# Performance work log

Hardware: AMD Instinct MI355X
Metric: run time of the kernel (lower is better)

Reference implementation:

```python
import jax, jax.numpy as jnp
import numpy as np

D_MODEL = 1024
NUM_HEADS = 16
DEPTH = D_MODEL // NUM_HEADS  # 64
BATCH = 4
SEQ = 2048


def _split_heads(x, batch):
    # [B, S, d_model] -> [B, H, S, depth]
    x = x.reshape(batch, -1, NUM_HEADS, DEPTH)
    return jnp.transpose(x, (0, 2, 1, 3))


def setup_inputs() -> dict:
    key = jax.random.key(0)
    ks = jax.random.split(key, 8)
    q = jax.random.normal(ks[0], (BATCH, SEQ, D_MODEL), jnp.float32)
    k = jax.random.normal(ks[1], (BATCH, SEQ, D_MODEL), jnp.float32)
    v = jax.random.normal(ks[2], (BATCH, SEQ, D_MODEL), jnp.float32)
    scale = 0.02
    wq = jax.random.normal(ks[3], (D_MODEL, D_MODEL), jnp.float32) * scale
    wk = jax.random.normal(ks[4], (D_MODEL, D_MODEL), jnp.float32) * scale
    wv = jax.random.normal(ks[5], (D_MODEL, D_MODEL), jnp.float32) * scale
    wo = jax.random.normal(ks[6], (D_MODEL, D_MODEL), jnp.float32) * scale
    zeros_b = jnp.zeros((D_MODEL,), jnp.float32)
    ones_mask = jnp.ones((BATCH, SEQ, 1), jnp.float32)
    return {
        "q": q, "k": k, "v": v,
        "query_mask": ones_mask, "key_mask": ones_mask, "value_mask": ones_mask,
        "wq": wq, "bq": zeros_b, "wk": wk, "bk": zeros_b,
        "wv": wv, "bv": zeros_b, "wo": wo, "bo": zeros_b,
    }


def reference(q, k, v, query_mask, key_mask, value_mask,
              wq, bq, wk, bk, wv, bv, wo, bo):
    batch, q_len, _ = q.shape
    # elementwise input masks (multiplicative, as in the original call())
    q = q * query_mask
    k = k * key_mask
    v = v * value_mask
    # linear projections + head split
    qh = _split_heads(q @ wq + bq, batch)  # [B, H, Q, depth]
    kh = _split_heads(k @ wk + bk, batch)  # [B, H, S, depth]
    vh = _split_heads(v @ wv + bv, batch)  # [B, H, S, depth]
    key_len = kh.shape[2]
    layout_length = key_len // NUM_HEADS  # L
    # The TF slice_assign loop uses full slices on every axis, so each
    # iteration overwrites the whole buffer; after the loop only the LAST
    # head-block slice survives. Faithful math:
    start = (NUM_HEADS - 1) * layout_length
    fk = kh[:, :, start:start + layout_length, :]  # [B, H, L, depth]
    fv = vh[:, :, start:start + layout_length, :]  # [B, H, L, depth]
    dk = jnp.asarray(DEPTH, jnp.float32)
    logits = jnp.einsum("bhqd,bhld->bhql", qh, fk) / jnp.sqrt(dk)
    # autoreg mask: 1 - lower_triangular(ones(Q, L)) -> strictly upper masked
    tri = jnp.tril(jnp.ones((q_len, layout_length), jnp.float32))
    mask = (1.0 - tri)[None, None, :, :]
    logits = logits + mask * (-1e9)
    attn = jax.nn.softmax(logits, axis=-1)  # [B, H, Q, L]
    out = jnp.einsum("bhql,bhld->bhqd", attn, fv)  # [B, H, Q, depth]
    out = jnp.transpose(out, (0, 2, 1, 3)).reshape(batch, -1, D_MODEL)
    output = out @ wo + bo
    return (output, attn)
```

## Files before the change

kernel.cpp:

```cpp
#include <hip/hip_runtime.h>

typedef unsigned short u16;
typedef unsigned int u32;
typedef __attribute__((ext_vector_type(8))) short short8;
typedef __attribute__((ext_vector_type(4))) short short4v;
typedef __attribute__((ext_vector_type(4))) float f32x4;

__device__ __forceinline__ u16 f2bf(float f) {
  union { float f; u32 u; } v; v.f = f;
  u32 u = v.u;
  u32 r = (u + 0x7fffu + ((u >> 16) & 1u)) >> 16;
  return (u16)r;
}

__device__ __forceinline__ void async_ld16(const u16* g, u16* l) {
  __builtin_amdgcn_global_load_lds(
      (const __attribute__((address_space(1))) void*)g,
      (__attribute__((address_space(3))) void*)l, 16, 0, 0);
}

__global__ __launch_bounds__(256) void prep(
    const float* __restrict__ q, const float* __restrict__ qm,
    const float* __restrict__ k, const float* __restrict__ km,
    const float* __restrict__ v, const float* __restrict__ vm,
    const float* __restrict__ wq, const float* __restrict__ wk,
    const float* __restrict__ wv, const float* __restrict__ wo,
    u16* __restrict__ Qc, u16* __restrict__ Kc, u16* __restrict__ Vc,
    u16* __restrict__ WqT, u16* __restrict__ WkT, u16* __restrict__ WvT,
    u16* __restrict__ WoT) {
  __shared__ u16 tile[32][33];
  const int bid = blockIdx.x;
  const int tid = threadIdx.x;
  if (bid < 8192) {
    int i = (bid * 256 + tid) * 4;
    float m = qm[i >> 10];
    float4 vv = *(const float4*)(q + i);
    short4v o;
    o.x = (short)f2bf(vv.x * m);
    o.y = (short)f2bf(vv.y * m);
    o.z = (short)f2bf(vv.z * m);
    o.w = (short)f2bf(vv.w * m);
    *(short4v*)(Qc + i) = o;
  } else if (bid < 9216) {
    int zb = bid - 8192;
    int z = zb >> 9;
    int bx = zb & 511;
    const float* src = z ? v : k;
    const float* mask = z ? vm : km;
    u16* dst = z ? Vc : Kc;
    int i = (bx * 256 + tid) * 4;
    int r = i >> 10, c = i & 1023;
    size_t sr = (size_t)(r >> 7) * 2048 + 1920 + (r & 127);
    float m = mask[sr];
    float4 vv = *(const float4*)(src + sr * 1024 + c);
    short4v o;
    o.x = (short)f2bf(vv.x * m);
    o.y = (short)f2bf(vv.y * m);
    o.z = (short)f2bf(vv.z * m);
    o.w = (short)f2bf(vv.w * m);
    *(short4v*)(dst + i) = o;
  } else {
    int idx = bid - 9216;
    int z = idx >> 10;
    int rem = idx & 1023;
    const float* W = (z == 0) ? wq : (z == 1) ? wk : (z == 2) ? wv : wo;
    u16* WT = (z == 0) ? WqT : (z == 1) ? WkT : (z == 2) ? WvT : WoT;
    int tx = tid & 31, ty = tid >> 5;
    int x = (rem & 31) * 32 + tx;
    int y0 = (rem >> 5) * 32;
    for (int i = ty; i < 32; i += 8)
      tile[i][tx] = f2bf(W[(size_t)(y0 + i) * 1024 + x]);
    __syncthreads();
    int x2 = y0 + tx;
    int r0 = (rem & 31) * 32;
    for (int i = ty; i < 32; i += 8)
      WT[(size_t)(r0 + i) * 1024 + x2] = tile[tx][i];
  }
}

template <int OUTMODE>
__device__ __forceinline__ void gemm_body(
    const u16* __restrict__ A, const u16* __restrict__ BT,
    const float* __restrict__ bias, void* __restrict__ Cv, int N, int K,
    int bx, int by) {
  __shared__ u16 As[128 * 32];
  __shared__ u16 Bs[128 * 32];
  const int wave = threadIdx.x >> 6, lane = threadIdx.x & 63;
  const int ln = lane & 15, quad = lane >> 4;
  const int w0 = wave & 1, w1 = wave >> 1;
  const int row0 = bx * 128;
  const int col0 = by * 128;
  const int srow = lane >> 2, scol = (lane & 3) * 8;
  const u16* gA = A + (size_t)(row0 + wave * 32 + srow) * K + scol;
  const u16* gB = BT + (size_t)(col0 + wave * 32 + srow) * K + scol;
  u16* lA = &As[(wave * 32) * 32];
  u16* lB = &Bs[(wave * 32) * 32];

  f32x4 acc[4][4];
  for (int i = 0; i < 4; ++i)
    for (int j = 0; j < 4; ++j) acc[i][j] = f32x4{0.f, 0.f, 0.f, 0.f};

  for (int k0 = 0; k0 < K; k0 += 32) {
    async_ld16(gA + k0, lA);
    async_ld16(gA + (size_t)16 * K + k0, lA + 16 * 32);
    async_ld16(gB + k0, lB);
    async_ld16(gB + (size_t)16 * K + k0, lB + 16 * 32);
    __syncthreads();
    short8 af[4], bf[4];
    for (int mt = 0; mt < 4; ++mt)
      af[mt] = *(const short8*)&As[(w1 * 64 + mt * 16 + ln) * 32 + quad * 8];
    for (int nt = 0; nt < 4; ++nt)
      bf[nt] = *(const short8*)&Bs[(w0 * 64 + nt * 16 + ln) * 32 + quad * 8];
    for (int mt = 0; mt < 4; ++mt)
      for (int nt = 0; nt < 4; ++nt)
        acc[mt][nt] = __builtin_amdgcn_mfma_f32_16x16x32_bf16(af[mt], bf[nt],
                                                              acc[mt][nt], 0, 0, 0);
    __syncthreads();
  }

  for (int nt = 0; nt < 4; ++nt) {
    int c = col0 + w0 * 64 + nt * 16 + ln;
    float bval = bias ? bias[c] : 0.f;
    for (int mt = 0; mt < 4; ++mt)
      for (int reg = 0; reg < 4; ++reg) {
        int r = row0 + w1 * 64 + mt * 16 + quad * 4 + reg;
        float val = acc[mt][nt][reg] + bval;
        if (OUTMODE == 3) {
          ((float*)Cv)[(size_t)r * N + c] = val;
        } else if (OUTMODE == 0) {
          ((u16*)Cv)[(size_t)r * N + c] = f2bf(val);
        } else if (OUTMODE == 1) {
          size_t idx = ((size_t)(r >> 7) << 17) + ((size_t)(c >> 6) << 13) +
                       ((size_t)(r & 127) << 6) + (c & 63);
          ((u16*)Cv)[idx] = f2bf(val);
        } else {
          size_t idx = ((size_t)(r >> 7) << 17) + ((size_t)(c >> 6) << 13) +
                       ((size_t)(c & 63) << 7) + (r & 127);
          ((u16*)Cv)[idx] = f2bf(val);
        }
      }
  }
}

__global__ __launch_bounds__(256) void proj(
    const u16* __restrict__ Qc, const u16* __restrict__ Kc,
    const u16* __restrict__ Vc, const u16* __restrict__ WqT,
    const u16* __restrict__ WkT, const u16* __restrict__ WvT,
    const float* __restrict__ bq, const float* __restrict__ bk,
    const float* __restrict__ bv, u16* __restrict__ Qws, u16* __restrict__ FK,
    u16* __restrict__ FVT) {
  int orig = blockIdx.x;
  int id = (orig & 7) * 72 + (orig >> 3);
  if (id < 512) {
    gemm_body<0>(Qc, WqT, bq, Qws, 1024, 1024, id >> 3, id & 7);
  } else if (id < 544) {
    int t = id - 512;
    gemm_body<1>(Kc, WkT, bk, FK, 1024, 1024, t >> 3, t & 7);
  } else {
    int t = id - 544;
    gemm_body<2>(Vc, WvT, bv, FVT, 1024, 1024, t >> 3, t & 7);
  }
}

__global__ __launch_bounds__(256) void gemm_o(const u16* __restrict__ A,
                                              const u16* __restrict__ BT,
                                              const float* __restrict__ bias,
                                              float* __restrict__ C) {
  int orig = blockIdx.x;
  int id = (orig & 7) * 64 + (orig >> 3);
  gemm_body<3>(A, BT, bias, C, 1024, 1024, id >> 3, id & 7);
}

__global__ __launch_bounds__(256) void attn_kernel(
    const u16* __restrict__ Q, const u16* __restrict__ FK,
    const u16* __restrict__ FVT, float* __restrict__ attn_out,
    u16* __restrict__ OUTP) {
  __shared__ u16 pbuf[4][16 * 136];
  const int wave = threadIdx.x >> 6, lane = threadIdx.x & 63;
  const int ln = lane & 15, quad = lane >> 4;
  const int bh = blockIdx.x, b = bh >> 4, h = bh & 15;
  const int q0 = blockIdx.y * 64 + wave * 16;

  const u16* qp = Q + (size_t)(b * 2048 + q0 + ln) * 1024 + h * 64 + quad * 8;
  const u16* fk = FK + ((size_t)bh << 13);
  const u16* fvt = FVT + ((size_t)bh << 13);

  f32x4 acc[8];
  for (int i = 0; i < 8; ++i) acc[i] = f32x4{0.f, 0.f, 0.f, 0.f};
  for (int ks = 0; ks < 2; ++ks) {
    short8 a = *(const short8*)(qp + ks * 32);
    __builtin_amdgcn_s_setprio(1);
    for (int nt = 0; nt < 8; ++nt) {
      short8 bfrag = *(const short8*)(fk + (size_t)(nt * 16 + ln) * 64 +
                                      ks * 32 + quad * 8);
      acc[nt] = __builtin_amdgcn_mfma_f32_16x16x32_bf16(a, bfrag, acc[nt], 0, 0, 0);
    }
    __builtin_amdgcn_s_setprio(0);
  }
  float mx[4] = {-3e38f, -3e38f, -3e38f, -3e38f};
  for (int nt = 0; nt < 8; ++nt) {
    int l = nt * 16 + ln;
    for (int reg = 0; reg < 4; ++reg) {
      int qg = q0 + quad * 4 + reg;
      float vv = acc[nt][reg] * 0.125f;
      if (l > qg) vv = -1e9f;
      acc[nt][reg] = vv;
      mx[reg] = fmaxf(mx[reg], vv);
    }
  }
  for (int off = 1; off < 16; off <<= 1)
    for (int reg = 0; reg < 4; ++reg)
      mx[reg] = fmaxf(mx[reg], __shfl_xor(mx[reg], off, 64));
  float sm[4] = {0.f, 0.f, 0.f, 0.f};
  for (int nt = 0; nt < 8; ++nt)
    for (int reg = 0; reg < 4; ++reg) {
      float p = __expf(acc[nt][reg] - mx[reg]);
      acc[nt][reg] = p;
      sm[reg] += p;
    }
  for (int off = 1; off < 16; off <<= 1)
    for (int reg = 0; reg < 4; ++reg) sm[reg] += __shfl_xor(sm[reg], off, 64);
  float inv[4];
  for (int reg = 0; reg < 4; ++reg) inv[reg] = 1.f / sm[reg];
  {
    float* ao = attn_out + ((size_t)bh * 2048 + q0 + quad * 4) * 128 + ln;
    u16* pw = &pbuf[wave][(quad * 4) * 136 + ln];
    for (int nt = 0; nt < 8; ++nt)
      for (int reg = 0; reg < 4; ++reg) {
        float pv = acc[nt][reg] * inv[reg];
        ao[(size_t)reg * 128 + nt * 16] = pv;
        pw[reg * 136 + nt * 16] = f2bf(pv);
      }
  }
  f32x4 o[4];
  for (int i = 0; i < 4; ++i) o[i] = f32x4{0.f, 0.f, 0.f, 0.f};
  for (int kk = 0; kk < 4; ++kk) {
    short8 a = *(const short8*)&pbuf[wave][ln * 136 + kk * 32 + quad * 8];
    __builtin_amdgcn_s_setprio(1);
    for (int nt = 0; nt < 4; ++nt) {
      short8 bfrag = *(const short8*)(fvt + (size_t)(nt * 16 + ln) * 128 +
                                      kk * 32 + quad * 8);
      o[nt] = __builtin_amdgcn_mfma_f32_16x16x32_bf16(a, bfrag, o[nt], 0, 0, 0);
    }
    __builtin_amdgcn_s_setprio(0);
  }
  {
    u16* ot = &pbuf[wave][0];
    for (int nt = 0; nt < 4; ++nt)
      for (int reg = 0; reg < 4; ++reg)
        ot[(quad * 4 + reg) * 72 + nt * 16 + ln] = f2bf(o[nt][reg]);
    int row = lane >> 2;
    u16* dst = OUTP + (size_t)(b * 2048 + q0 + row) * 1024 + h * 64;
    for (int p = 0; p < 2; ++p) {
      int col = p * 32 + (lane & 3) * 8;
      *(short8*)(dst + col) = *(const short8*)&ot[row * 72 + col];
    }
  }
}

extern "C" void kernel_launch(void* const* d_in, const int* in_sizes, int n_in,
                              void* d_out, int out_size, void* d_ws,
                              size_t ws_size, hipStream_t stream) {
  const float* q = (const float*)d_in[0];
  const float* k = (const float*)d_in[1];
  const float* v = (const float*)d_in[2];
  const float* qm = (const float*)d_in[3];
  const float* km = (const float*)d_in[4];
  const float* vm = (const float*)d_in[5];
  const float* wq = (const float*)d_in[6];
  const float* bq = (const float*)d_in[7];
  const float* wk = (const float*)d_in[8];
  const float* bk = (const float*)d_in[9];
  const float* wv = (const float*)d_in[10];
  const float* bv = (const float*)d_in[11];
  const float* wo = (const float*)d_in[12];
  const float* bo = (const float*)d_in[13];
  float* out = (float*)d_out;
  float* attn_out = out + (size_t)4 * 2048 * 1024;

  char* ws = (char*)d_ws;
  const size_t MB = 1ull << 20;
  u16* WqT = (u16*)(ws + 0 * MB);
  u16* WkT = (u16*)(ws + 2 * MB);
  u16* WvT = (u16*)(ws + 4 * MB);
  u16* WoT = (u16*)(ws + 6 * MB);
  u16* Qws = (u16*)(ws + 8 * MB);
  u16* FKw = (u16*)(ws + 24 * MB);
  u16* FVTw = (u16*)(ws + 25 * MB);
  u16* OUTP = (u16*)(ws + 26 * MB);
  u16* Qc = OUTP;
  u16* Kc = (u16*)(ws + 42 * MB);
  u16* Vc = (u16*)(ws + 43 * MB);

  prep<<<13312, 256, 0, stream>>>(q, qm, k, km, v, vm, wq, wk, wv, wo, Qc, Kc,
                                  Vc, WqT, WkT, WvT, WoT);
  proj<<<576, 256, 0, stream>>>(Qc, Kc, Vc, WqT, WkT, WvT, bq, bk, bv, Qws,
                                FKw, FVTw);
  attn_kernel<<<dim3(64, 32), 256, 0, stream>>>(Qws, FKw, FVTw, attn_out, OUTP);
  gemm_o<<<512, 256, 0, stream>>>(OUTP, WoT, bo, out);
}
```

Before: 284.6 us.

## Fuse Q projection with attention via LDS tile and atomic flag for K/V readiness

Merges the projection and attention kernels into one launch: each block computes a 128x128 Q-projection tile into shared memory and immediately runs attention for the two heads and 64-row groups it covers, so the Q intermediate never goes through global memory. The first 64 blocks additionally compute the K/V last-slice projections and signal completion through an atomic counter that all blocks spin on. This removes a kernel launch and the Q write/readback, but puts extra serial work on the first 64 blocks. It also relies on all 512 blocks being co-resident or the K/V producers being scheduled first; otherwise the spin-wait can deadlock.

```diff
diff --git a/kernel.cpp b/kernel.cpp
--- a/kernel.cpp
+++ b/kernel.cpp
@@ -82,9 +82,7 @@
 __device__ __forceinline__ void gemm_body(
     const u16* __restrict__ A, const u16* __restrict__ BT,
     const float* __restrict__ bias, void* __restrict__ Cv, int N, int K,
-    int bx, int by) {
-  __shared__ u16 As[128 * 32];
-  __shared__ u16 Bs[128 * 32];
+    int bx, int by, u16* __restrict__ As, u16* __restrict__ Bs) {
   const int wave = threadIdx.x >> 6, lane = threadIdx.x & 63;
   const int ln = lane & 15, quad = lane >> 4;
   const int w0 = wave & 1, w1 = wave >> 1;
@@ -127,38 +125,151 @@
         float val = acc[mt][nt][reg] + bval;
         if (OUTMODE == 3) {
           ((float*)Cv)[(size_t)r * N + c] = val;
-        } else if (OUTMODE == 0) {
-          ((u16*)Cv)[(size_t)r * N + c] = f2bf(val);
         } else if (OUTMODE == 1) {
           size_t idx = ((size_t)(r >> 7) << 17) + ((size_t)(c >> 6) << 13) +
                        ((size_t)(r & 127) << 6) + (c & 63);
           ((u16*)Cv)[idx] = f2bf(val);
-        } else {
+        } else if (OUTMODE == 2) {
           size_t idx = ((size_t)(r >> 7) << 17) + ((size_t)(c >> 6) << 13) +
                        ((size_t)(c & 63) << 7) + (r & 127);
           ((u16*)Cv)[idx] = f2bf(val);
+        } else {
+          ((u16*)Cv)[wave * 4608 + (mt * 16 + quad * 4 + reg) * 72 +
+                     nt * 16 + ln] = f2bf(val);
         }
       }
   }
 }
 
-__global__ __launch_bounds__(256) void proj(
+__global__ __launch_bounds__(256, 2) void proj_attn(
     const u16* __restrict__ Qc, const u16* __restrict__ Kc,
     const u16* __restrict__ Vc, const u16* __restrict__ WqT,
     const u16* __restrict__ WkT, const u16* __restrict__ WvT,
     const float* __restrict__ bq, const float* __restrict__ bk,
-    const float* __restrict__ bv, u16* __restrict__ Qws, u16* __restrict__ FK,
-    u16* __restrict__ FVT) {
-  int orig = blockIdx.x;
-  int id = (orig & 7) * 72 + (orig >> 3);
-  if (id < 512) {
-    gemm_body<0>(Qc, WqT, bq, Qws, 1024, 1024, id >> 3, id & 7);
-  } else if (id < 544) {
-    int t = id - 512;
-    gemm_body<1>(Kc, WkT, bk, FK, 1024, 1024, t >> 3, t & 7);
-  } else {
-    int t = id - 544;
-    gemm_body<2>(Vc, WvT, bv, FVT, 1024, 1024, t >> 3, t & 7);
+    const float* __restrict__ bv, u16* __restrict__ FK, u16* __restrict__ FVT,
+    float* __restrict__ attn_out, u16* __restrict__ OUTP,
+    u32* __restrict__ flags) {
+  __shared__ u16 As[128 * 32];
+  __shared__ u16 Bs[128 * 32];
+  __shared__ u16 qt_s[4 * 4608];
+  __shared__ u16 p_s[4 * 2176];
+  const int bid = blockIdx.x;
+  const int wave = threadIdx.x >> 6, lane = threadIdx.x & 63;
+  const int ln = lane & 15, quad = lane >> 4;
+
+  if (bid < 64) {
+    int z = bid >> 5, t = bid & 31;
+    if (z == 0)
+      gemm_body<1>(Kc, WkT, bk, FK, 1024, 1024, t >> 3, t & 7, As, Bs);
+    else
+      gemm_body<2>(Vc, WvT, bv, FVT, 1024, 1024, t >> 3, t & 7, As, Bs);
+    __syncthreads();
+    __threadfence();
+    if (threadIdx.x == 0)
+      __hip_atomic_fetch_add(flags, 1u, __ATOMIC_RELEASE,
+                             __HIP_MEMORY_SCOPE_AGENT);
+    __syncthreads();
+  }
+
+  int id = (bid & 7) * 64 + (bid >> 3);
+  const int bx = id >> 3, by = id & 7;
+  gemm_body<4>(Qc, WqT, bq, (void*)qt_s, 1024, 1024, bx, by, As, Bs);
+
+  if (threadIdx.x == 0) {
+    while (__hip_atomic_load(flags, __ATOMIC_ACQUIRE,
+                             __HIP_MEMORY_SCOPE_AGENT) < 64u)
+      __builtin_amdgcn_s_sleep(8);
+  }
+  __syncthreads();
+  __threadfence();
+
+  const int w0 = wave & 1, w1 = wave >> 1;
+  const int h = 2 * by + w0;
+  const int rowbase = bx * 128 + w1 * 64;
+  const int b = rowbase >> 11, q0 = rowbase & 2047;
+  const int bh = b * 16 + h;
+  const u16* qt = &qt_s[wave * 4608];
+  u16* pb = &p_s[wave * 2176];
+  const u16* fk = FK + ((size_t)bh << 13);
+  const u16* fvt = FVT + ((size_t)bh << 13);
+
+  for (int amt = 0; amt < 4; ++amt) {
+    const int qbase = q0 + amt * 16;
+    f32x4 acc[8];
+    for (int i = 0; i < 8; ++i) acc[i] = f32x4{0.f, 0.f, 0.f, 0.f};
+    for (int ks = 0; ks < 2; ++ks) {
+      short8 a =
+          *(const short8*)&qt[(amt * 16 + ln) * 72 + ks * 32 + quad * 8];
+      __builtin_amdgcn_s_setprio(1);
+      for (int nt = 0; nt < 8; ++nt) {
+        short8 bfrag = *(const short8*)(fk + (size_t)(nt * 16 + ln) * 64 +
+                                        ks * 32 + quad * 8);
+        acc[nt] =
+            __builtin_amdgcn_mfma_f32_16x16x32_bf16(a, bfrag, acc[nt], 0, 0, 0);
+      }
+      __builtin_amdgcn_s_setprio(0);
+    }
+    float mx[4] = {-3e38f, -3e38f, -3e38f, -3e38f};
+    for (int nt = 0; nt < 8; ++nt) {
+      int l = nt * 16 + ln;
+      for (int reg = 0; reg < 4; ++reg) {
+        int qg = qbase + quad * 4 + reg;
+        float vv = acc[nt][reg] * 0.125f;
+        if (l > qg) vv = -1e9f;
+        acc[nt][reg] = vv;
+        mx[reg] = fmaxf(mx[reg], vv);
+      }
+    }
+    for (int off = 1; off < 16; off <<= 1)
+      for (int reg = 0; reg < 4; ++reg)
+        mx[reg] = fmaxf(mx[reg], __shfl_xor(mx[reg], off, 64));
+    float sm[4] = {0.f, 0.f, 0.f, 0.f};
+    for (int nt = 0; nt < 8; ++nt)
+      for (int reg = 0; reg < 4; ++reg) {
+        float p = __expf(acc[nt][reg] - mx[reg]);
+        acc[nt][reg] = p;
+        sm[reg] += p;
+      }
+    for (int off = 1; off < 16; off <<= 1)
+      for (int reg = 0; reg < 4; ++reg) sm[reg] += __shfl_xor(sm[reg], off, 64);
+    float inv[4];
+    for (int reg = 0; reg < 4; ++reg) inv[reg] = 1.f / sm[reg];
+    {
+      float* ao =
+          attn_out + ((size_t)bh * 2048 + qbase + quad * 4) * 128 + ln;
+      u16* pw = &pb[(quad * 4) * 136 + ln];
+      for (int nt = 0; nt < 8; ++nt)
+        for (int reg = 0; reg < 4; ++reg) {
+          float pv = acc[nt][reg] * inv[reg];
+          ao[(size_t)reg * 128 + nt * 16] = pv;
+          pw[reg * 136 + nt * 16] = f2bf(pv);
+        }
+    }
+    f32x4 o[4];
+    for (int i = 0; i < 4; ++i) o[i] = f32x4{0.f, 0.f, 0.f, 0.f};
+    for (int kk = 0; kk < 4; ++kk) {
+      short8 a = *(const short8*)&pb[ln * 136 + kk * 32 + quad * 8];
+      __builtin_amdgcn_s_setprio(1);
+      for (int nt = 0; nt < 4; ++nt) {
+        short8 bfrag = *(const short8*)(fvt + (size_t)(nt * 16 + ln) * 128 +
+                                        kk * 32 + quad * 8);
+        o[nt] =
+            __builtin_amdgcn_mfma_f32_16x16x32_bf16(a, bfrag, o[nt], 0, 0, 0);
+      }
+      __builtin_amdgcn_s_setprio(0);
+    }
+    {
+      u16* ot = pb;
+      for (int nt = 0; nt < 4; ++nt)
+        for (int reg = 0; reg < 4; ++reg)
+          ot[(quad * 4 + reg) * 72 + nt * 16 + ln] = f2bf(o[nt][reg]);
+      int row = lane >> 2;
+      u16* dst = OUTP + (size_t)(b * 2048 + qbase + row) * 1024 + h * 64;
+      for (int p = 0; p < 2; ++p) {
+        int col = p * 32 + (lane & 3) * 8;
+        *(short8*)(dst + col) = *(const short8*)&ot[row * 72 + col];
+      }
+    }
   }
 }
 
@@ -166,96 +277,11 @@
                                               const u16* __restrict__ BT,
                                               const float* __restrict__ bias,
                                               float* __restrict__ C) {
+  __shared__ u16 As[128 * 32];
+  __shared__ u16 Bs[128 * 32];
   int orig = blockIdx.x;
   int id = (orig & 7) * 64 + (orig >> 3);
-  gemm_body<3>(A, BT, bias, C, 1024, 1024, id >> 3, id & 7);
-}
-
-__global__ __launch_bounds__(256) void attn_kernel(
-    const u16* __restrict__ Q, const u16* __restrict__ FK,
-    const u16* __restrict__ FVT, float* __restrict__ attn_out,
-    u16* __restrict__ OUTP) {
-  __shared__ u16 pbuf[4][16 * 136];
-  const int wave = threadIdx.x >> 6, lane = threadIdx.x & 63;
-  const int ln = lane & 15, quad = lane >> 4;
-  const int bh = blockIdx.x, b = bh >> 4, h = bh & 15;
-  const int q0 = blockIdx.y * 64 + wave * 16;
-
-  const u16* qp = Q + (size_t)(b * 2048 + q0 + ln) * 1024 + h * 64 + quad * 8;
-  const u16* fk = FK + ((size_t)bh << 13);
-  const u16* fvt = FVT + ((size_t)bh << 13);
-
-  f32x4 acc[8];
-  for (int i = 0; i < 8; ++i) acc[i] = f32x4{0.f, 0.f, 0.f, 0.f};
-  for (int ks = 0; ks < 2; ++ks) {
-    short8 a = *(const short8*)(qp + ks * 32);
-    __builtin_amdgcn_s_setprio(1);
-    for (int nt = 0; nt < 8; ++nt) {
-      short8 bfrag = *(const short8*)(fk + (size_t)(nt * 16 + ln) * 64 +
-                                      ks * 32 + quad * 8);
-      acc[nt] = __builtin_amdgcn_mfma_f32_16x16x32_bf16(a, bfrag, acc[nt], 0, 0, 0);
-    }
-    __builtin_amdgcn_s_setprio(0);
-  }
-  float mx[4] = {-3e38f, -3e38f, -3e38f, -3e38f};
-  for (int nt = 0; nt < 8; ++nt) {
-    int l = nt * 16 + ln;
-    for (int reg = 0; reg < 4; ++reg) {
-      int qg = q0 + quad * 4 + reg;
-      float vv = acc[nt][reg] * 0.125f;
-      if (l > qg) vv = -1e9f;
-      acc[nt][reg] = vv;
-      mx[reg] = fmaxf(mx[reg], vv);
-    }
-  }
-  for (int off = 1; off < 16; off <<= 1)
-    for (int reg = 0; reg < 4; ++reg)
-      mx[reg] = fmaxf(mx[reg], __shfl_xor(mx[reg], off, 64));
-  float sm[4] = {0.f, 0.f, 0.f, 0.f};
-  for (int nt = 0; nt < 8; ++nt)
-    for (int reg = 0; reg < 4; ++reg) {
-      float p = __expf(acc[nt][reg] - mx[reg]);
-      acc[nt][reg] = p;
-      sm[reg] += p;
-    }
-  for (int off = 1; off < 16; off <<= 1)
-    for (int reg = 0; reg < 4; ++reg) sm[reg] += __shfl_xor(sm[reg], off, 64);
-  float inv[4];
-  for (int reg = 0; reg < 4; ++reg) inv[reg] = 1.f / sm[reg];
-  {
-    float* ao = attn_out + ((size_t)bh * 2048 + q0 + quad * 4) * 128 + ln;
-    u16* pw = &pbuf[wave][(quad * 4) * 136 + ln];
-    for (int nt = 0; nt < 8; ++nt)
-      for (int reg = 0; reg < 4; ++reg) {
-        float pv = acc[nt][reg] * inv[reg];
-        ao[(size_t)reg * 128 + nt * 16] = pv;
-        pw[reg * 136 + nt * 16] = f2bf(pv);
-      }
-  }
-  f32x4 o[4];
-  for (int i = 0; i < 4; ++i) o[i] = f32x4{0.f, 0.f, 0.f, 0.f};
-  for (int kk = 0; kk < 4; ++kk) {
-    short8 a = *(const short8*)&pbuf[wave][ln * 136 + kk * 32 + quad * 8];
-    __builtin_amdgcn_s_setprio(1);
-    for (int nt = 0; nt < 4; ++nt) {
-      short8 bfrag = *(const short8*)(fvt + (size_t)(nt * 16 + ln) * 128 +
-                                      kk * 32 + quad * 8);
-      o[nt] = __builtin_amdgcn_mfma_f32_16x16x32_bf16(a, bfrag, o[nt], 0, 0, 0);
-    }
-    __builtin_amdgcn_s_setprio(0);
-  }
-  {
-    u16* ot = &pbuf[wave][0];
-    for (int nt = 0; nt < 4; ++nt)
-      for (int reg = 0; reg < 4; ++reg)
-        ot[(quad * 4 + reg) * 72 + nt * 16 + ln] = f2bf(o[nt][reg]);
-    int row = lane >> 2;
-    u16* dst = OUTP + (size_t)(b * 2048 + q0 + row) * 1024 + h * 64;
-    for (int p = 0; p < 2; ++p) {
-      int col = p * 32 + (lane & 3) * 8;
-      *(short8*)(dst + col) = *(const short8*)&ot[row * 72 + col];
-    }
-  }
+  gemm_body<3>(A, BT, bias, C, 1024, 1024, id >> 3, id & 7, As, Bs);
 }
 
 extern "C" void kernel_launch(void* const* d_in, const int* in_sizes, int n_in,
@@ -284,18 +310,18 @@
   u16* WkT = (u16*)(ws + 2 * MB);
   u16* WvT = (u16*)(ws + 4 * MB);
   u16* WoT = (u16*)(ws + 6 * MB);
-  u16* Qws = (u16*)(ws + 8 * MB);
   u16* FKw = (u16*)(ws + 24 * MB);
   u16* FVTw = (u16*)(ws + 25 * MB);
   u16* OUTP = (u16*)(ws + 26 * MB);
-  u16* Qc = OUTP;
-  u16* Kc = (u16*)(ws + 42 * MB);
-  u16* Vc = (u16*)(ws + 43 * MB);
-
+  u16* Qc = (u16*)(ws + 44 * MB);
+  u16* Kc = (u16*)(ws + 60 * MB);
+  u16* Vc = (u16*)(ws + 61 * MB);
+  u32* flags = (u32*)(ws + 62 * MB);
+
+  hipMemsetAsync(flags, 0, 4, stream);
   prep<<<13312, 256, 0, stream>>>(q, qm, k, km, v, vm, wq, wk, wv, wo, Qc, Kc,
                                   Vc, WqT, WkT, WvT, WoT);
-  proj<<<576, 256, 0, stream>>>(Qc, Kc, Vc, WqT, WkT, WvT, bq, bk, bv, Qws,
-                                FKw, FVTw);
-  attn_kernel<<<dim3(64, 32), 256, 0, stream>>>(Qws, FKw, FVTw, attn_out, OUTP);
+  proj_attn<<<512, 256, 0, stream>>>(Qc, Kc, Vc, WqT, WkT, WvT, bq, bk, bv,
+                                     FKw, FVTw, attn_out, OUTP, flags);
   gemm_o<<<512, 256, 0, stream>>>(OUTP, WoT, bo, out);
 }
```

Result: slower. 364.6 us (+28.1%).
